# Performance work log

Hardware: AMD Instinct MI355X
Metric: run time of the kernel (lower is better)

## Reference

```python
import jax, jax.numpy as jnp
import numpy as np

B, F, C, O, M = 128, 4096, 32, 32, 9  # batch, num_fields, in_ch, out_ch, num_coeffs (moves incl. self)


def setup_inputs() -> dict:
    key = jax.random.key(0)
    k1, k2, k3, k4 = jax.random.split(key, 4)
    x = jax.random.normal(k1, (B, F, C), dtype=jnp.float32)
    # mask[m, f] = index of the source field feeding target field f via move m
    mask = jax.random.randint(k2, (M, F), 0, F, dtype=jnp.int32)
    init_std = 1.0 / (3.0 * np.sqrt(C * O))  # matches TruncatedNormal stddev in build()
    conv_coeffs = jax.random.normal(k3, (M, C, O), dtype=jnp.float32) * init_std
    # biases are zero-initialized in the original; use small random values so the
    # bias-add path is exercised numerically
    biases = jax.random.normal(k4, (F, O), dtype=jnp.float32) * 0.01
    return {"x": x, "mask": mask, "conv_coeffs": conv_coeffs, "biases": biases}


def reference(x, mask, conv_coeffs, biases):
    # ch_convolve_by_moves: gather source fields per move, per-move matmul, per-field bias.
    # gathered[b, m, f, c] = x[b, mask[m, f], c]
    gathered = jnp.take(x, mask, axis=1)              # [B, M, F, C]
    out = jnp.einsum('bmfc,mco->bfo', gathered, conv_coeffs)  # sum over moves and in-channels
    return out + biases                               # per-field bias broadcast over batch
```

## Files before the change

### kernel.cpp

```cpp
#include <hip/hip_runtime.h>


#define B_ 128
#define F_ 4096
#define C_ 32
#define O_ 32
#define M_ 9
#define T_ 18
#define TF1 32
#define LROW1 528

typedef _Float16 halfx4 __attribute__((ext_vector_type(4)));
typedef _Float16 halfx8 __attribute__((ext_vector_type(8)));
typedef float floatx4 __attribute__((ext_vector_type(4)));
typedef float floatx16 __attribute__((ext_vector_type(16)));

__global__ __launch_bounds__(256) void pass1_transpose(
    const float* __restrict__ x, const float* __restrict__ coeffs,
    _Float16* __restrict__ xh, _Float16* __restrict__ wf)
{
    __shared__ _Float16 tile[TF1 * LROW1];
    const int blk = blockIdx.x;
    const int bs  = blk & 7;
    const int f0  = (blk >> 3) * TF1;
    const int tid = threadIdx.x;

    {
        const int f_l = tid >> 3;
        const int c4  = (tid & 7) * 4;
        const float* src = x + ((size_t)f0 + f_l) * C_ + c4;
#pragma unroll
        for (int bp = 0; bp < 16; ++bp) {
            const floatx4* p = reinterpret_cast<const floatx4*>(
                src + (size_t)(bs * 16 + bp) * (F_ * C_));
            floatx4 v = __builtin_nontemporal_load(p);
            halfx4 hv;
            hv[0] = (_Float16)v[0]; hv[1] = (_Float16)v[1];
            hv[2] = (_Float16)v[2]; hv[3] = (_Float16)v[3];
            *reinterpret_cast<halfx4*>(&tile[f_l * LROW1 + bp * C_ + c4]) = hv;
        }
    }
    __syncthreads();

    {
        const int wv   = tid >> 6;
        const int lane = tid & 63;
#pragma unroll
        for (int it = 0; it < TF1 / 4; ++it) {
            int f_l = it * 4 + wv;
            halfx8 v = *reinterpret_cast<const halfx8*>(&tile[f_l * LROW1 + lane * 8]);
            *reinterpret_cast<halfx8*>(
                xh + ((size_t)bs * F_ + f0 + f_l) * (16 * C_) + lane * 8) = v;
        }
    }

    if (blk == 0) {
        for (int id = tid; id < T_ * 64; id += 256) {
            int t  = id >> 6;
            int L  = id & 63;
            int m  = t >> 1;
            int cb = 16 * (t & 1) + 8 * (L >> 5);
            int o  = L & 31;
            halfx8 w;
#pragma unroll
            for (int j = 0; j < 8; ++j)
                w[j] = (_Float16)coeffs[(m * C_ + cb + j) * O_ + o];
            *reinterpret_cast<halfx8*>(wf + id * 8) = w;
        }
    }
}

__global__ __launch_bounds__(256, 4) void pass2_gemm(
    const _Float16* __restrict__ xh, const _Float16* __restrict__ wf,
    const int* __restrict__ mask, const float* __restrict__ biases,
    float* __restrict__ out)
{
    __shared__ _Float16 sw[T_ * 64 * 8];
    const int tid = threadIdx.x;
#pragma unroll
    for (int i = tid; i < T_ * 64; i += 256)
        reinterpret_cast<halfx8*>(sw)[i] = reinterpret_cast<const halfx8*>(wf)[i];
    __syncthreads();

    const int blk  = blockIdx.x;
    const int bs   = blk & 7;
    const int fg   = blk >> 3;
    const int wave = tid >> 6;
    const int lane = tid & 63;
    const int h    = lane >> 5;
    const int row  = lane & 31;
    const int fi   = row >> 4;
    const int bp   = row & 15;
    const int ocol = lane & 31;

    const int fa = fg * 8 + 2 * wave;
    const int f  = fa + fi;

    const _Float16* xb = xh + (size_t)bs * F_ * (16 * C_) + bp * C_ + 8 * h;

    int sidx[M_];
#pragma unroll
    for (int m = 0; m < M_; ++m) sidx[m] = mask[m * F_ + f];

    halfx8 a[T_];
#pragma unroll
    for (int m = 0; m < M_; ++m) {
        const _Float16* rp = xb + (size_t)sidx[m] * (16 * C_);
        a[2 * m]     = *reinterpret_cast<const halfx8*>(rp);
        a[2 * m + 1] = *reinterpret_cast<const halfx8*>(rp + 16);
    }

    floatx16 acc;
#pragma unroll
    for (int i = 0; i < 16; ++i) acc[i] = 0.0f;
#pragma unroll
    for (int t = 0; t < T_; ++t) {
        halfx8 bwt = *reinterpret_cast<const halfx8*>(&sw[(t * 64 + lane) * 8]);
        acc = __builtin_amdgcn_mfma_f32_32x32x16_f16(a[t], bwt, acc, 0, 0, 0);
    }

    float bias_a = biases[(size_t)fa * O_ + ocol];
    float bias_b = biases[(size_t)(fa + 1) * O_ + ocol];
#pragma unroll
    for (int r = 0; r < 16; ++r) {
        int orow = (r & 3) + 8 * (r >> 2) + 4 * h;
        int ofi  = orow >> 4;
        int b    = bs * 16 + (orow & 15);
        float v  = acc[r] + (ofi ? bias_b : bias_a);
        __builtin_nontemporal_store(
            v, &out[((size_t)b * F_ + fa + ofi) * O_ + ocol]);
    }
}

__global__ __launch_bounds__(256) void fallback_kernel(
    const float* __restrict__ x, const int* __restrict__ mask,
    const float* __restrict__ coeffs, const float* __restrict__ biases,
    float* __restrict__ out)
{
    int gid = blockIdx.x * 256 + threadIdx.x;
    int o = gid & (O_ - 1);
    int f = (gid >> 5) & (F_ - 1);
    int b = gid >> 17;
    float acc = biases[f * O_ + o];
    for (int m = 0; m < M_; ++m) {
        int s = mask[m * F_ + f];
        const float* xr = x + ((size_t)b * F_ + s) * C_;
        const float* wr = coeffs + (m * C_) * O_ + o;
#pragma unroll
        for (int c = 0; c < C_; ++c)
            acc += xr[c] * wr[c * O_];
    }
    out[gid] = acc;
}

extern "C" void kernel_launch(void* const* d_in, const int* in_sizes, int n_in,
                              void* d_out, int out_size, void* d_ws, size_t ws_size,
                              hipStream_t stream) {
    const float* x      = (const float*)d_in[0];
    const int*   mask   = (const int*)d_in[1];
    const float* coeffs = (const float*)d_in[2];
    const float* biases = (const float*)d_in[3];
    float* out = (float*)d_out;

    const size_t xh_elems = (size_t)B_ * F_ * C_;
    const size_t need = xh_elems * sizeof(_Float16) + (size_t)T_ * 64 * 8 * sizeof(_Float16);

    if (ws_size >= need) {
        _Float16* xh = (_Float16*)d_ws;
        _Float16* wf = xh + xh_elems;
        pass1_transpose<<<8 * (F_ / TF1), 256, 0, stream>>>(x, coeffs, xh, wf);
        pass2_gemm<<<8 * (F_ / 8), 256, 0, stream>>>(xh, wf, mask, biases, out);
    } else {
        fallback_kernel<<<(B_ * F_ * O_) / 256, 256, 0, stream>>>(x, mask, coeffs, biases, out);
    }
}
```

Measured before the change: 143.5 us.

## Process more fields per block with double-buffered gather prefetch

```diff
diff --git a/kernel.cpp b/kernel.cpp
--- a/kernel.cpp
+++ b/kernel.cpp
@@ -9,6 +9,8 @@
 #define T_ 18
 #define TF1 32
 #define LROW1 528
+#define FPB2 64
+#define NIT 8
 
 typedef _Float16 halfx4 __attribute__((ext_vector_type(4)));
 typedef _Float16 halfx8 __attribute__((ext_vector_type(8)));
@@ -70,21 +72,24 @@
     }
 }
 
-__global__ __launch_bounds__(256, 4) void pass2_gemm(
+__global__ __launch_bounds__(256, 2) void pass2_gemm(
     const _Float16* __restrict__ xh, const _Float16* __restrict__ wf,
     const int* __restrict__ mask, const float* __restrict__ biases,
     float* __restrict__ out)
 {
     __shared__ _Float16 sw[T_ * 64 * 8];
+    __shared__ int smask[M_][FPB2];
     const int tid = threadIdx.x;
-#pragma unroll
+    const int blk = blockIdx.x;
+    const int bs  = blk & 7;
+    const int f0  = (blk >> 3) * FPB2;
+
     for (int i = tid; i < T_ * 64; i += 256)
         reinterpret_cast<halfx8*>(sw)[i] = reinterpret_cast<const halfx8*>(wf)[i];
+    for (int i = tid; i < M_ * FPB2; i += 256)
+        smask[i >> 6][i & 63] = mask[(i >> 6) * F_ + f0 + (i & 63)];
     __syncthreads();
 
-    const int blk  = blockIdx.x;
-    const int bs   = blk & 7;
-    const int fg   = blk >> 3;
     const int wave = tid >> 6;
     const int lane = tid & 63;
     const int h    = lane >> 5;
@@ -93,42 +98,51 @@
     const int bp   = row & 15;
     const int ocol = lane & 31;
 
-    const int fa = fg * 8 + 2 * wave;
-    const int f  = fa + fi;
-
     const _Float16* xb = xh + (size_t)bs * F_ * (16 * C_) + bp * C_ + 8 * h;
 
-    int sidx[M_];
+    halfx8 a[2][T_];
+    {
+        const int floc = 2 * wave + fi;
 #pragma unroll
-    for (int m = 0; m < M_; ++m) sidx[m] = mask[m * F_ + f];
-
-    halfx8 a[T_];
-#pragma unroll
-    for (int m = 0; m < M_; ++m) {
-        const _Float16* rp = xb + (size_t)sidx[m] * (16 * C_);
-        a[2 * m]     = *reinterpret_cast<const halfx8*>(rp);
-        a[2 * m + 1] = *reinterpret_cast<const halfx8*>(rp + 16);
+        for (int m = 0; m < M_; ++m) {
+            const _Float16* rp = xb + (size_t)smask[m][floc] * (16 * C_);
+            a[0][2 * m]     = *reinterpret_cast<const halfx8*>(rp);
+            a[0][2 * m + 1] = *reinterpret_cast<const halfx8*>(rp + 16);
+        }
     }
 
-    floatx16 acc;
 #pragma unroll
-    for (int i = 0; i < 16; ++i) acc[i] = 0.0f;
+    for (int it = 0; it < NIT; ++it) {
+        const int cur = it & 1;
+        if (it + 1 < NIT) {
+            const int floc = (it + 1) * 8 + 2 * wave + fi;
 #pragma unroll
-    for (int t = 0; t < T_; ++t) {
-        halfx8 bwt = *reinterpret_cast<const halfx8*>(&sw[(t * 64 + lane) * 8]);
-        acc = __builtin_amdgcn_mfma_f32_32x32x16_f16(a[t], bwt, acc, 0, 0, 0);
-    }
-
-    float bias_a = biases[(size_t)fa * O_ + ocol];
-    float bias_b = biases[(size_t)(fa + 1) * O_ + ocol];
+            for (int m = 0; m < M_; ++m) {
+                const _Float16* rp = xb + (size_t)smask[m][floc] * (16 * C_);
+                a[cur ^ 1][2 * m]     = *reinterpret_cast<const halfx8*>(rp);
+                a[cur ^ 1][2 * m + 1] = *reinterpret_cast<const halfx8*>(rp + 16);
+            }
+        }
+        floatx16 acc;
 #pragma unroll
-    for (int r = 0; r < 16; ++r) {
-        int orow = (r & 3) + 8 * (r >> 2) + 4 * h;
-        int ofi  = orow >> 4;
-        int b    = bs * 16 + (orow & 15);
-        float v  = acc[r] + (ofi ? bias_b : bias_a);
-        __builtin_nontemporal_store(
-            v, &out[((size_t)b * F_ + fa + ofi) * O_ + ocol]);
+        for (int i = 0; i < 16; ++i) acc[i] = 0.0f;
+#pragma unroll
+        for (int t = 0; t < T_; ++t) {
+            halfx8 bwt = *reinterpret_cast<const halfx8*>(&sw[(t * 64 + lane) * 8]);
+            acc = __builtin_amdgcn_mfma_f32_32x32x16_f16(a[cur][t], bwt, acc, 0, 0, 0);
+        }
+        const int fa = f0 + it * 8 + 2 * wave;
+        float bias_a = biases[(size_t)fa * O_ + ocol];
+        float bias_b = biases[(size_t)(fa + 1) * O_ + ocol];
+#pragma unroll
+        for (int r = 0; r < 16; ++r) {
+            int orow = (r & 3) + 8 * (r >> 2) + 4 * h;
+            int ofi  = orow >> 4;
+            int b    = bs * 16 + (orow & 15);
+            float v  = acc[r] + (ofi ? bias_b : bias_a);
+            __builtin_nontemporal_store(
+                v, &out[((size_t)b * F_ + fa + ofi) * O_ + ocol]);
+        }
     }
 }
 
@@ -169,7 +183,7 @@
         _Float16* xh = (_Float16*)d_ws;
         _Float16* wf = xh + xh_elems;
         pass1_transpose<<<8 * (F_ / TF1), 256, 0, stream>>>(x, coeffs, xh, wf);
-        pass2_gemm<<<8 * (F_ / 8), 256, 0, stream>>>(xh, wf, mask, biases, out);
+        pass2_gemm<<<8 * (F_ / FPB2), 256, 0, stream>>>(xh, wf, mask, biases, out);
     } else {
         fallback_kernel<<<(B_ * F_ * O_) / 256, 256, 0, stream>>>(x, mask, coeffs, biases, out);
     }
```

After: 153.6 us. +7.0%, slower.
